# Kernel tuning notes

Hardware: AMD Instinct MI355X
Metric: run time of the kernel (lower is better)

## Reference

```python
import jax, jax.numpy as jnp
import numpy as np

N_NODES = 50000
N_REL = 500
D = 128
N_EDGES = 600000


def setup_inputs() -> dict:
    key = jax.random.key(0)
    k1, k2, k3, k4, k5 = jax.random.split(key, 5)
    h = jax.random.normal(k1, (N_NODES, D), dtype=jnp.float32)
    g = jax.random.normal(k2, (N_REL, D), dtype=jnp.float32)
    row = jax.random.randint(k3, (N_EDGES,), 0, N_NODES)
    col = jax.random.randint(k4, (N_EDGES,), 0, N_NODES)
    edge_idx = jnp.stack([row, col], axis=0)  # [2, E]
    edge_type = jax.random.randint(k5, (N_EDGES,), 0, N_REL)
    return {"h": h, "g": g, "edge_idx": edge_idx, "edge_type": edge_type}


def reference(h, g, edge_idx, edge_type):
    # d = || h[row] + g[type] - h[col] ||_1 per edge  -> [E]
    row, col = edge_idx[0], edge_idx[1]
    diff = h[row] + g[edge_type] - h[col]  # [E, D] fused gather+combine
    return jnp.sum(jnp.abs(diff), axis=1)
```

## Files before the change

### kernel.cpp

```cpp
#include <hip/hip_runtime.h>
#include <hip/hip_fp16.h>


#define D 128
#define MAXREL 500
typedef float f32x2 __attribute__((ext_vector_type(2)));

__global__ void __launch_bounds__(256) KB_cvt(
    const float* __restrict__ h_in, unsigned int* __restrict__ h8, int n4_h,
    const float* __restrict__ g_in, unsigned int* __restrict__ g8, int n4_g)
{
    const int total = n4_h + n4_g;
    for (int i = blockIdx.x * 256 + threadIdx.x; i < total; i += gridDim.x * 256) {
        const bool isH = (i < n4_h);
        const int  j   = isH ? i : i - n4_h;
        const float4 v = isH ? reinterpret_cast<const float4*>(h_in)[j]
                             : reinterpret_cast<const float4*>(g_in)[j];
        unsigned int w = 0;
        w = __builtin_amdgcn_cvt_pk_fp8_f32(v.x, v.y, w, false);
        w = __builtin_amdgcn_cvt_pk_fp8_f32(v.z, v.w, w, true);
        (isH ? h8 : g8)[j] = w;
    }
}

__global__ void __launch_bounds__(1024) KB_main(
    const unsigned int* __restrict__ h8,
    const unsigned int* __restrict__ g8,
    const int* __restrict__ eidx,
    const int* __restrict__ etype,
    float* __restrict__ out,
    int E, int ng_u4, int niter)
{
    __shared__ unsigned int gs[MAXREL * (D / 4)];

    {
        uint4* gsv = reinterpret_cast<uint4*>(gs);
        const uint4* gv = reinterpret_cast<const uint4*>(g8);
        for (int i = threadIdx.x; i < ng_u4; i += 1024) gsv[i] = gv[i];
    }
    __syncthreads();

    const int grp = threadIdx.x >> 3;
    const int sub = threadIdx.x & 7;

    for (int it = blockIdx.x; it < niter; it += gridDim.x) {
        const int e0 = it * 512 + grp * 4;
        if (e0 >= E) continue;

        int r[4], c[4], t[4];
        #pragma unroll
        for (int k = 0; k < 4; ++k) {
            const int e = min(e0 + k, E - 1);
            r[k] = eidx[e];
            c[k] = eidx[E + e];
            t[k] = etype[e];
        }

        uint4 hr[4], hc[4];
        #pragma unroll
        for (int k = 0; k < 4; ++k)
            hr[k] = *reinterpret_cast<const uint4*>(h8 + (size_t)r[k] * 32 + sub * 4);
        #pragma unroll
        for (int k = 0; k < 4; ++k)
            hc[k] = *reinterpret_cast<const uint4*>(h8 + (size_t)c[k] * 32 + sub * 4);

        uint4 gw[4];
        #pragma unroll
        for (int k = 0; k < 4; ++k)
            gw[k] = *reinterpret_cast<const uint4*>(gs + t[k] * 32 + sub * 4);

        float s0 = 0.f, s1 = 0.f, s2 = 0.f, s3 = 0.f;
        #pragma unroll
        for (int k = 0; k < 4; ++k) {
            const unsigned int ha[4] = {hr[k].x, hr[k].y, hr[k].z, hr[k].w};
            const unsigned int hb[4] = {hc[k].x, hc[k].y, hc[k].z, hc[k].w};
            const unsigned int gg[4] = {gw[k].x, gw[k].y, gw[k].z, gw[k].w};
            float s = 0.f;
            #pragma unroll
            for (int j = 0; j < 4; ++j) {
                const f32x2 a0 = __builtin_amdgcn_cvt_pk_f32_fp8(ha[j], false);
                const f32x2 a1 = __builtin_amdgcn_cvt_pk_f32_fp8(ha[j], true);
                const f32x2 c0 = __builtin_amdgcn_cvt_pk_f32_fp8(hb[j], false);
                const f32x2 c1 = __builtin_amdgcn_cvt_pk_f32_fp8(hb[j], true);
                const f32x2 g0 = __builtin_amdgcn_cvt_pk_f32_fp8(gg[j], false);
                const f32x2 g1 = __builtin_amdgcn_cvt_pk_f32_fp8(gg[j], true);
                s += fabsf(a0.x + g0.x - c0.x) + fabsf(a0.y + g0.y - c0.y)
                   + fabsf(a1.x + g1.x - c1.x) + fabsf(a1.y + g1.y - c1.y);
            }
            s += __shfl_xor(s, 4, 8);
            s += __shfl_xor(s, 2, 8);
            s += __shfl_xor(s, 1, 8);
            if (k == 0) s0 = s; else if (k == 1) s1 = s; else if (k == 2) s2 = s; else s3 = s;
        }

        const float v = (sub == 0) ? s0 : (sub == 1) ? s1 : (sub == 2) ? s2 : s3;
        if (sub < 4 && e0 + sub < E) out[e0 + sub] = v;
    }
}

__global__ void __launch_bounds__(256) KB_transe_l1_f32(
    const float* __restrict__ h, const float* __restrict__ g,
    const int* __restrict__ eidx, const int* __restrict__ etype,
    float* __restrict__ out, int E)
{
    const int tid  = blockIdx.x * 256 + threadIdx.x;
    const int edge = tid >> 5;
    const int lane = threadIdx.x & 31;
    if (edge >= E) return;
    const int r = eidx[edge], c = eidx[E + edge], t = etype[edge];
    const int d = lane * 4;
    const float4 hr = *reinterpret_cast<const float4*>(h + (size_t)r * D + d);
    const float4 hc = *reinterpret_cast<const float4*>(h + (size_t)c * D + d);
    const float4 gt = *reinterpret_cast<const float4*>(g + (size_t)t * D + d);
    float s = fabsf(hr.x + gt.x - hc.x) + fabsf(hr.y + gt.y - hc.y)
            + fabsf(hr.z + gt.z - hc.z) + fabsf(hr.w + gt.w - hc.w);
    #pragma unroll
    for (int o = 16; o >= 1; o >>= 1) s += __shfl_xor(s, o, 32);
    if (lane == 0) out[edge] = s;
}

extern "C" void kernel_launch(void* const* d_in, const int* in_sizes, int n_in,
                              void* d_out, int out_size, void* d_ws, size_t ws_size,
                              hipStream_t stream) {
    const float* h     = (const float*)d_in[0];
    const float* g     = (const float*)d_in[1];
    const int*   eidx  = (const int*)d_in[2];
    const int*   etype = (const int*)d_in[3];
    float*       out   = (float*)d_out;

    const int E   = in_sizes[3];
    const int n_h = in_sizes[0];
    const int n_g = in_sizes[1];

    const size_t need = (size_t)n_h + (size_t)n_g;
    const bool ok = (n_g / D) <= MAXREL && (n_g % 16 == 0) && (n_h % D == 0);

    if (ws_size >= need && ok) {
        unsigned int* h8 = (unsigned int*)d_ws;
        unsigned int* g8 = (unsigned int*)((char*)d_ws + (size_t)n_h);
        const int n4_h = n_h / 4, n4_g = n_g / 4;
        const int cgrid = (n4_h + n4_g + 255) / 256;
        KB_cvt<<<cgrid, 256, 0, stream>>>(h, h8, n4_h, g, g8, n4_g);

        const int niter = (E + 511) / 512;
        KB_main<<<512, 1024, 0, stream>>>(h8, g8, eidx, etype, out, E, n_g / 16, niter);
    } else {
        const long long threads = (long long)E * 32;
        const int grid = (int)((threads + 255) / 256);
        KB_transe_l1_f32<<<grid, 256, 0, stream>>>(h, g, eidx, etype, out, E);
    }
}
```

Before: 31.35 us.

## Split fp8 embedding table into column halves and process in two passes

The conversion kernel now writes the fp8 h and g tables as two separate half-width arrays, one for the low 64 columns and one for the high 64. The main kernel runs twice, once per half, so each pass gathers from a 3.2 MB table that is more likely to stay cache-resident, and the second pass accumulates into the output. Edge indices are loaded coalesced, one per thread, and broadcast with shuffles, and loads and stores use nontemporal hints. The cost is reading the index arrays twice, an extra read-modify-write of the output, and one more kernel launch.

```diff
diff --git a/kernel.cpp b/kernel.cpp
--- a/kernel.cpp
+++ b/kernel.cpp
@@ -1,14 +1,15 @@
 #include <hip/hip_runtime.h>
-#include <hip/hip_fp16.h>
 
 
 #define D 128
 #define MAXREL 500
 typedef float f32x2 __attribute__((ext_vector_type(2)));
 
-__global__ void __launch_bounds__(256) KB_cvt(
-    const float* __restrict__ h_in, unsigned int* __restrict__ h8, int n4_h,
-    const float* __restrict__ g_in, unsigned int* __restrict__ g8, int n4_g)
+__global__ void __launch_bounds__(256) KB_cvt_split(
+    const float* __restrict__ h_in, unsigned int* __restrict__ h8lo,
+    unsigned int* __restrict__ h8hi, int n4_h,
+    const float* __restrict__ g_in, unsigned int* __restrict__ g8lo,
+    unsigned int* __restrict__ g8hi, int n4_g)
 {
     const int total = n4_h + n4_g;
     for (int i = blockIdx.x * 256 + threadIdx.x; i < total; i += gridDim.x * 256) {
@@ -19,62 +20,63 @@
         unsigned int w = 0;
         w = __builtin_amdgcn_cvt_pk_fp8_f32(v.x, v.y, w, false);
         w = __builtin_amdgcn_cvt_pk_fp8_f32(v.z, v.w, w, true);
-        (isH ? h8 : g8)[j] = w;
+        const int row = j >> 5;
+        const int p   = j & 31;
+        unsigned int* dst = isH ? (p < 16 ? h8lo : h8hi)
+                                : (p < 16 ? g8lo : g8hi);
+        dst[row * 16 + (p & 15)] = w;
     }
 }
 
-__global__ void __launch_bounds__(1024) KB_main(
+template <int PASS>
+__global__ void __launch_bounds__(512, 6) KB_half(
     const unsigned int* __restrict__ h8,
-    const unsigned int* __restrict__ g8,
+    const unsigned int* __restrict__ g8h,
     const int* __restrict__ eidx,
     const int* __restrict__ etype,
     float* __restrict__ out,
-    int E, int ng_u4, int niter)
+    int E, int ng_u4h, int nchunks)
 {
-    __shared__ unsigned int gs[MAXREL * (D / 4)];
+    __shared__ unsigned int gs[MAXREL * 16];
 
     {
         uint4* gsv = reinterpret_cast<uint4*>(gs);
-        const uint4* gv = reinterpret_cast<const uint4*>(g8);
-        for (int i = threadIdx.x; i < ng_u4; i += 1024) gsv[i] = gv[i];
+        const uint4* gv = reinterpret_cast<const uint4*>(g8h);
+        for (int i = threadIdx.x; i < ng_u4h; i += 512) gsv[i] = gv[i];
     }
     __syncthreads();
 
-    const int grp = threadIdx.x >> 3;
-    const int sub = threadIdx.x & 7;
+    const int sub   = threadIdx.x & 3;
+    const int lbase = (threadIdx.x & 63) & ~3;
 
-    for (int it = blockIdx.x; it < niter; it += gridDim.x) {
-        const int e0 = it * 512 + grp * 4;
-        if (e0 >= E) continue;
+    for (int it = blockIdx.x; it < nchunks; it += gridDim.x) {
+        const int base = it * 512;
+        if (base >= E) continue;
+        const int e_me = min(base + (int)threadIdx.x, E - 1);
 
-        int r[4], c[4], t[4];
+        const int r_me = __builtin_nontemporal_load(eidx + e_me);
+        const int c_me = __builtin_nontemporal_load(eidx + E + e_me);
+        const int t_me = __builtin_nontemporal_load(etype + e_me);
+        float prev = 0.f;
+        if (PASS == 1) prev = __builtin_nontemporal_load(out + e_me);
+
+        uint4 hr[4], hc[4]; unsigned int tt[4];
         #pragma unroll
         for (int k = 0; k < 4; ++k) {
-            const int e = min(e0 + k, E - 1);
-            r[k] = eidx[e];
-            c[k] = eidx[E + e];
-            t[k] = etype[e];
+            const int rk = __shfl(r_me, lbase + k, 64);
+            const int ck = __shfl(c_me, lbase + k, 64);
+            tt[k] = (unsigned)__shfl(t_me, lbase + k, 64);
+            hr[k] = *reinterpret_cast<const uint4*>(h8 + (size_t)rk * 16 + sub * 4);
+            hc[k] = *reinterpret_cast<const uint4*>(h8 + (size_t)ck * 16 + sub * 4);
         }
-
-        uint4 hr[4], hc[4];
-        #pragma unroll
-        for (int k = 0; k < 4; ++k)
-            hr[k] = *reinterpret_cast<const uint4*>(h8 + (size_t)r[k] * 32 + sub * 4);
-        #pragma unroll
-        for (int k = 0; k < 4; ++k)
-            hc[k] = *reinterpret_cast<const uint4*>(h8 + (size_t)c[k] * 32 + sub * 4);
-
-        uint4 gw[4];
-        #pragma unroll
-        for (int k = 0; k < 4; ++k)
-            gw[k] = *reinterpret_cast<const uint4*>(gs + t[k] * 32 + sub * 4);
 
         float s0 = 0.f, s1 = 0.f, s2 = 0.f, s3 = 0.f;
         #pragma unroll
         for (int k = 0; k < 4; ++k) {
+            const uint4 gw = *reinterpret_cast<const uint4*>(gs + tt[k] * 16 + sub * 4);
             const unsigned int ha[4] = {hr[k].x, hr[k].y, hr[k].z, hr[k].w};
             const unsigned int hb[4] = {hc[k].x, hc[k].y, hc[k].z, hc[k].w};
-            const unsigned int gg[4] = {gw[k].x, gw[k].y, gw[k].z, gw[k].w};
+            const unsigned int gg[4] = {gw.x, gw.y, gw.z, gw.w};
             float s = 0.f;
             #pragma unroll
             for (int j = 0; j < 4; ++j) {
@@ -87,14 +89,14 @@
                 s += fabsf(a0.x + g0.x - c0.x) + fabsf(a0.y + g0.y - c0.y)
                    + fabsf(a1.x + g1.x - c1.x) + fabsf(a1.y + g1.y - c1.y);
             }
-            s += __shfl_xor(s, 4, 8);
-            s += __shfl_xor(s, 2, 8);
-            s += __shfl_xor(s, 1, 8);
+            s += __shfl_xor(s, 2, 4);
+            s += __shfl_xor(s, 1, 4);
             if (k == 0) s0 = s; else if (k == 1) s1 = s; else if (k == 2) s2 = s; else s3 = s;
         }
 
         const float v = (sub == 0) ? s0 : (sub == 1) ? s1 : (sub == 2) ? s2 : s3;
-        if (sub < 4 && e0 + sub < E) out[e0 + sub] = v;
+        if (base + (int)threadIdx.x < E)
+            __builtin_nontemporal_store((PASS == 1) ? prev + v : v, out + e_me);
     }
 }
 
@@ -133,17 +135,22 @@
     const int n_g = in_sizes[1];
 
     const size_t need = (size_t)n_h + (size_t)n_g;
-    const bool ok = (n_g / D) <= MAXREL && (n_g % 16 == 0) && (n_h % D == 0);
+    const bool ok = (n_g / D) <= MAXREL && (n_g % (2 * D) == 0) && (n_h % (2 * D) == 0);
 
     if (ws_size >= need && ok) {
-        unsigned int* h8 = (unsigned int*)d_ws;
-        unsigned int* g8 = (unsigned int*)((char*)d_ws + (size_t)n_h);
+        unsigned int* h8lo = (unsigned int*)d_ws;
+        unsigned int* h8hi = (unsigned int*)((char*)d_ws + (size_t)n_h / 2);
+        unsigned int* g8lo = (unsigned int*)((char*)d_ws + (size_t)n_h);
+        unsigned int* g8hi = (unsigned int*)((char*)d_ws + (size_t)n_h + (size_t)n_g / 2);
+
         const int n4_h = n_h / 4, n4_g = n_g / 4;
         const int cgrid = (n4_h + n4_g + 255) / 256;
-        KB_cvt<<<cgrid, 256, 0, stream>>>(h, h8, n4_h, g, g8, n4_g);
+        KB_cvt_split<<<cgrid, 256, 0, stream>>>(h, h8lo, h8hi, n4_h, g, g8lo, g8hi, n4_g);
 
-        const int niter = (E + 511) / 512;
-        KB_main<<<512, 1024, 0, stream>>>(h8, g8, eidx, etype, out, E, n_g / 16, niter);
+        const int ng_u4h = n_g / 2 / 16;
+        const int nchunks = (E + 511) / 512;
+        KB_half<0><<<768, 512, 0, stream>>>(h8lo, g8lo, eidx, etype, out, E, ng_u4h, nchunks);
+        KB_half<1><<<768, 512, 0, stream>>>(h8hi, g8hi, eidx, etype, out, E, ng_u4h, nchunks);
     } else {
         const long long threads = (long long)E * 32;
         const int grid = (int)((threads + 255) / 256);
```

Measured after the change: 39.39 us. 25.7% more time.
